# Performance work log

Measured on AMD Instinct MI355X. Metric: run time of the kernel, lower is better.

The kernel has to match this reference:

```python
import jax, jax.numpy as jnp
import numpy as np

B, IN_DIM, OUT_DIM, DEGREE = 4096, 1024, 1024, 4
LN_EPS = 1e-5


def setup_inputs() -> dict:
    key = jax.random.key(0)
    k_x, k_c = jax.random.split(key)
    x = jax.random.normal(k_x, (B, IN_DIM), dtype=jnp.float32)
    # xavier_normal_ on tensor of shape (in, out, deg+1): fan_in/fan_out from
    # torch convention: fan_in = out*(deg+1)? torch computes fan_in=size(1)*receptive,
    # for 3D tensor fan_in = shape[1]*shape[2], fan_out = shape[0]*shape[2].
    fan_in = OUT_DIM * (DEGREE + 1)
    fan_out = IN_DIM * (DEGREE + 1)
    std = float(np.sqrt(2.0 / (fan_in + fan_out)))
    cheby_coeffs = jax.random.normal(k_c, (IN_DIM, OUT_DIM, DEGREE + 1), dtype=jnp.float32) * std
    ln_weight = jnp.ones((IN_DIM,), dtype=jnp.float32)
    ln_bias = jnp.zeros((IN_DIM,), dtype=jnp.float32)
    return {"x": x, "cheby_coeffs": cheby_coeffs, "ln_weight": ln_weight, "ln_bias": ln_bias}


def _layer_norm(x, w, b):
    mu = jnp.mean(x, axis=-1, keepdims=True)
    var = jnp.mean(jnp.square(x - mu), axis=-1, keepdims=True)
    return (x - mu) * jax.lax.rsqrt(var + LN_EPS) * w + b


def reference(x, cheby_coeffs, ln_weight, ln_bias):
    h = jnp.tanh(_layer_norm(x, ln_weight, ln_bias))  # [B, I]
    # Chebyshev recurrence T0=1, T1=h, T_{n}=2h*T_{n-1}-T_{n-2}
    cheby = [jnp.ones_like(h), h]
    for _ in range(2, DEGREE + 1):
        cheby.append(2.0 * h * cheby[-1] - cheby[-2])
    stacked = jnp.stack(cheby, axis=-1)  # [B, I, D+1]
    y = jnp.einsum('bid,iod->bo', stacked, cheby_coeffs)
    return jax.nn.silu(y)
```

## Files before the change

kernel.cpp:

```cpp
#include <hip/hip_runtime.h>
#include <cstdint>
#include <cstddef>

#define BATCH 4096
#define IDIM 1024
#define ODIM 1024
#define KDIM 4096
#define KHALF 2048

typedef __attribute__((ext_vector_type(8))) short bf16x8;
typedef __attribute__((ext_vector_type(4))) float f32x4;

__device__ __forceinline__ unsigned short f2bf(float f) {
  union { float f; unsigned int u; } v; v.f = f;
  unsigned int r = (v.u + 0x7FFFu + ((v.u >> 16) & 1u)) >> 16;
  return (unsigned short)r;
}
__device__ __forceinline__ float bf2f(unsigned short u) {
  union { unsigned int u; float f; } v; v.u = ((unsigned int)u) << 16;
  return v.f;
}

__device__ __forceinline__ void load_lds16(const void* g, void* l) {
  __builtin_amdgcn_global_load_lds(
      (const __attribute__((address_space(1))) void*)g,
      (__attribute__((address_space(3))) void*)l, 16, 0, 0);
}

__device__ __forceinline__ int sidx(int p, int ii) {
  return p * 64 + ((ii + 4 * (p & 15)) & 63);
}

__global__ __launch_bounds__(256) void prep(
    const float* __restrict__ x, const float* __restrict__ lnw,
    const float* __restrict__ lnb, const float* __restrict__ C,
    unsigned short* __restrict__ A, unsigned short* __restrict__ Bt,
    float* __restrict__ biasPart) {
  __shared__ __align__(16) unsigned short sm[64 * 5 * 64];
  int bid = blockIdx.x;
  int t = threadIdx.x;

  if (bid < BATCH) {
    float* rs = (float*)sm;
    float* rq = ((float*)sm) + 4;
    const float4 v = ((const float4*)(x + (size_t)bid * IDIM))[t];
    float s  = v.x + v.y + v.z + v.w;
    float s2 = v.x * v.x + v.y * v.y + v.z * v.z + v.w * v.w;
#pragma unroll
    for (int off = 32; off > 0; off >>= 1) {
      s  += __shfl_down(s, off);
      s2 += __shfl_down(s2, off);
    }
    int lane = t & 63, wv = t >> 6;
    if (lane == 0) { rs[wv] = s; rq[wv] = s2; }
    __syncthreads();
    float S1 = rs[0] + rs[1] + rs[2] + rs[3];
    float S2 = rq[0] + rq[1] + rq[2] + rq[3];
    float mean = S1 * (1.0f / IDIM);
    float var  = S2 * (1.0f / IDIM) - mean * mean;
    float rstd = rsqrtf(var + 1e-5f);

    const float4 w4 = ((const float4*)lnw)[t];
    const float4 b4 = ((const float4*)lnb)[t];
    float xs[4]  = {v.x, v.y, v.z, v.w};
    float ws4[4] = {w4.x, w4.y, w4.z, w4.w};
    float bs4[4] = {b4.x, b4.y, b4.z, b4.w};

    unsigned short u1[4], u2[4], u3[4], u4[4];
#pragma unroll
    for (int j = 0; j < 4; j++) {
      float h  = tanhf((xs[j] - mean) * rstd * ws4[j] + bs4[j]);
      float T2 = 2.0f * h * h - 1.0f;
      float T3 = 2.0f * h * T2 - h;
      float T4 = 2.0f * h * T3 - T2;
      u1[j] = f2bf(h); u2[j] = f2bf(T2); u3[j] = f2bf(T3); u4[j] = f2bf(T4);
    }
    size_t base = (size_t)bid * KDIM;
    *(ushort4*)(A + base + 0 * IDIM + t * 4) = *(ushort4*)u1;
    *(ushort4*)(A + base + 1 * IDIM + t * 4) = *(ushort4*)u2;
    *(ushort4*)(A + base + 2 * IDIM + t * 4) = *(ushort4*)u3;
    *(ushort4*)(A + base + 3 * IDIM + t * 4) = *(ushort4*)u4;
  } else {
    int cb = bid - BATCH;
    int i0 = (cb & 15) * 64, o0 = (cb >> 4) * 64;
#pragma unroll
    for (int r = 0; r < 20; r++) {
      int idx = r * 256 + t;
      int ii  = idx / 80;
      int c4  = idx - ii * 80;
      const float4 f = *(const float4*)(C + ((size_t)(i0 + ii) * ODIM + o0) * 5 + c4 * 4);
      float vals[4] = {f.x, f.y, f.z, f.w};
#pragma unroll
      for (int j = 0; j < 4; j++) {
        int p = c4 * 4 + j;
        sm[sidx(p, ii)] = f2bf(vals[j]);
      }
    }
    __syncthreads();
#pragma unroll
    for (int r = 0; r < 16; r++) {
      int idx = r * 256 + t;
      int seg = idx >> 4, l16 = idx & 15;
      int oo = seg >> 2, d2 = seg & 3;
      int p = oo * 5 + d2 + 1;
      const unsigned short* src = &sm[sidx(p, l16 * 4)];
      ushort4 u = *(const ushort4*)src;
      *(ushort4*)(Bt + (size_t)(o0 + oo) * KDIM + d2 * IDIM + i0 + l16 * 4) = u;
    }
    if (t < 64) {
      float s = 0.f;
      int p = t * 5;
#pragma unroll
      for (int ii = 0; ii < 64; ii++) s += bf2f(sm[sidx(p, ii)]);
      biasPart[(size_t)(i0 >> 6) * ODIM + o0 + t] = s;
    }
  }
}

#define BM 128
#define BN 128
#define BK 64

__global__ __launch_bounds__(256, 2) void gemm_part(
    const unsigned short* __restrict__ A,
    const unsigned short* __restrict__ Bt,
    const float* __restrict__ biasPart,
    float* __restrict__ out0,
    float* __restrict__ part1) {
  __shared__ unsigned short As[BM * BK];
  __shared__ unsigned short Bs[BN * BK];
  int t = threadIdx.x;
  int lane = t & 63, w = t >> 6;
  int m0 = blockIdx.x * BM;
  int n0 = blockIdx.y * BN;
  size_t kbase = (size_t)blockIdx.z * KHALF;

  f32x4 acc[4][4];
#pragma unroll
  for (int i = 0; i < 4; i++)
#pragma unroll
    for (int j = 0; j < 4; j++) acc[i][j] = (f32x4){0.f, 0.f, 0.f, 0.f};

  int wm = (w >> 1) * 64;
  int wn = (w & 1) * 64;

  int sr = lane >> 3;
  int sc = ((lane & 7) ^ sr) * 8;
  const unsigned short* ag[4]; unsigned short* al[4];
  const unsigned short* bg[4]; unsigned short* bl[4];
#pragma unroll
  for (int q = 0; q < 4; q++) {
    int row = w * 8 + q * 32;
    ag[q] = A  + (size_t)(m0 + row + sr) * KDIM + kbase + sc;
    al[q] = &As[row * BK];
    bg[q] = Bt + (size_t)(n0 + row + sr) * KDIM + kbase + sc;
    bl[q] = &Bs[row * BK];
  }

  int arow = (wm + (lane & 15)) * BK;
  int brow = (wn + (lane & 15)) * BK;
  int x7 = lane & 7, hi = lane >> 4;

  for (int k0 = 0; k0 < KHALF; k0 += BK) {
#pragma unroll
    for (int q = 0; q < 4; q++) load_lds16(ag[q] + k0, al[q]);
#pragma unroll
    for (int q = 0; q < 4; q++) load_lds16(bg[q] + k0, bl[q]);
    __syncthreads();
#pragma unroll
    for (int kk = 0; kk < 2; kk++) {
      int co = ((kk * 4 + hi) ^ x7) * 8;
      bf16x8 af[4], bfv[4];
#pragma unroll
      for (int i = 0; i < 4; i++) af[i]  = *(const bf16x8*)&As[arow + i * 16 * BK + co];
#pragma unroll
      for (int j = 0; j < 4; j++) bfv[j] = *(const bf16x8*)&Bs[brow + j * 16 * BK + co];
#pragma unroll
      for (int i = 0; i < 4; i++)
#pragma unroll
        for (int j = 0; j < 4; j++)
          acc[i][j] = __builtin_amdgcn_mfma_f32_16x16x32_bf16(af[i], bfv[j], acc[i][j], 0, 0, 0);
    }
    __syncthreads();
  }

  float* dst = (blockIdx.z == 0) ? out0 : part1;
  bool addb = (blockIdx.z == 0);
#pragma unroll
  for (int j = 0; j < 4; j++) {
    int col = n0 + wn + j * 16 + (lane & 15);
    float bc = 0.f;
    if (addb) {
#pragma unroll
      for (int ib = 0; ib < 16; ib++) bc += biasPart[(size_t)ib * ODIM + col];
    }
#pragma unroll
    for (int i = 0; i < 4; i++) {
      int row = m0 + wm + i * 16 + hi * 4;
#pragma unroll
      for (int r = 0; r < 4; r++)
        dst[(size_t)(row + r) * ODIM + col] = acc[i][j][r] + bc;
    }
  }
}

__global__ __launch_bounds__(256) void reduce_silu(
    float* __restrict__ out, const float* __restrict__ part1) {
  int idx = blockIdx.x * 256 + threadIdx.x;
  float4 a = ((const float4*)out)[idx];
  float4 b = ((const float4*)part1)[idx];
  float y0 = a.x + b.x, y1 = a.y + b.y, y2 = a.z + b.z, y3 = a.w + b.w;
  float4 o;
  o.x = y0 / (1.0f + __expf(-y0));
  o.y = y1 / (1.0f + __expf(-y1));
  o.z = y2 / (1.0f + __expf(-y2));
  o.w = y3 / (1.0f + __expf(-y3));
  ((float4*)out)[idx] = o;
}

extern "C" void kernel_launch(void* const* d_in, const int* in_sizes, int n_in,
                              void* d_out, int out_size, void* d_ws, size_t ws_size,
                              hipStream_t stream) {
  const float* x    = (const float*)d_in[0];
  const float* coef = (const float*)d_in[1];
  const float* lnw  = (const float*)d_in[2];
  const float* lnb  = (const float*)d_in[3];
  float* out = (float*)d_out;

  char* ws = (char*)d_ws;
  unsigned short* A  = (unsigned short*)ws;
  unsigned short* Bt = (unsigned short*)(ws + (size_t)BATCH * KDIM * 2);
  char* p = ws + (size_t)BATCH * KDIM * 2 + (size_t)ODIM * KDIM * 2;
  float* biasPart = (float*)p;
  float* part1 = (float*)(p + 16 * ODIM * sizeof(float));

  prep<<<BATCH + 256, 256, 0, stream>>>(x, lnw, lnb, coef, A, Bt, biasPart);
  gemm_part<<<dim3(BATCH / BM, ODIM / BN, 2), 256, 0, stream>>>(A, Bt, biasPart, out, part1);
  reduce_silu<<<(BATCH * ODIM) / (256 * 4), 256, 0, stream>>>(out, part1);
}
```

Baseline: 138.9 us.

## Double-buffer LDS tiles in split-K GEMM to overlap global loads with MFMA

The GEMM main loop now uses two LDS buffers per operand. It issues the global-to-LDS loads for the next K tile before computing on the current one, so memory latency overlaps with MFMA work instead of stalling at each barrier. This doubles LDS use per block to 64KB, which may limit occupancy for the two-blocks-per-CU launch bound. Correctness depends on the __syncthreads making the async global_load_lds data visible, since there is no explicit vmcnt wait.

```diff
diff --git a/kernel.cpp b/kernel.cpp
--- a/kernel.cpp
+++ b/kernel.cpp
@@ -120,6 +120,7 @@
 #define BM 128
 #define BN 128
 #define BK 64
+#define NIT (KHALF / BK)
 
 __global__ __launch_bounds__(256, 2) void gemm_part(
     const unsigned short* __restrict__ A,
@@ -127,8 +128,8 @@
     const float* __restrict__ biasPart,
     float* __restrict__ out0,
     float* __restrict__ part1) {
-  __shared__ unsigned short As[BM * BK];
-  __shared__ unsigned short Bs[BN * BK];
+  __shared__ unsigned short As[2 * BM * BK];
+  __shared__ unsigned short Bs[2 * BN * BK];
   int t = threadIdx.x;
   int lane = t & 63, w = t >> 6;
   int m0 = blockIdx.x * BM;
@@ -161,27 +162,43 @@
   int brow = (wn + (lane & 15)) * BK;
   int x7 = lane & 7, hi = lane >> 4;
 
-  for (int k0 = 0; k0 < KHALF; k0 += BK) {
-#pragma unroll
-    for (int q = 0; q < 4; q++) load_lds16(ag[q] + k0, al[q]);
-#pragma unroll
-    for (int q = 0; q < 4; q++) load_lds16(bg[q] + k0, bl[q]);
-    __syncthreads();
-#pragma unroll
-    for (int kk = 0; kk < 2; kk++) {
-      int co = ((kk * 4 + hi) ^ x7) * 8;
-      bf16x8 af[4], bfv[4];
-#pragma unroll
-      for (int i = 0; i < 4; i++) af[i]  = *(const bf16x8*)&As[arow + i * 16 * BK + co];
-#pragma unroll
-      for (int j = 0; j < 4; j++) bfv[j] = *(const bf16x8*)&Bs[brow + j * 16 * BK + co];
-#pragma unroll
-      for (int i = 0; i < 4; i++)
-#pragma unroll
-        for (int j = 0; j < 4; j++)
-          acc[i][j] = __builtin_amdgcn_mfma_f32_16x16x32_bf16(af[i], bfv[j], acc[i][j], 0, 0, 0);
-    }
-    __syncthreads();
+#define ISSUE(buf, kk0)                                                     \
+  do {                                                                      \
+    int _k = (kk0);                                                         \
+    _Pragma("unroll")                                                       \
+    for (int q = 0; q < 4; q++) load_lds16(ag[q] + _k, al[q] + (buf) * (BM * BK)); \
+    _Pragma("unroll")                                                       \
+    for (int q = 0; q < 4; q++) load_lds16(bg[q] + _k, bl[q] + (buf) * (BN * BK)); \
+  } while (0)
+
+#define COMPUTE(buf)                                                        \
+  do {                                                                      \
+    _Pragma("unroll")                                                       \
+    for (int kk = 0; kk < 2; kk++) {                                        \
+      int co = ((kk * 4 + hi) ^ x7) * 8;                                    \
+      bf16x8 af[4], bfv[4];                                                 \
+      _Pragma("unroll")                                                     \
+      for (int i = 0; i < 4; i++)                                           \
+        af[i]  = *(const bf16x8*)&As[(buf) * (BM * BK) + arow + i * 16 * BK + co]; \
+      _Pragma("unroll")                                                     \
+      for (int j = 0; j < 4; j++)                                           \
+        bfv[j] = *(const bf16x8*)&Bs[(buf) * (BN * BK) + brow + j * 16 * BK + co]; \
+      _Pragma("unroll")                                                     \
+      for (int i = 0; i < 4; i++)                                           \
+        _Pragma("unroll")                                                   \
+        for (int j = 0; j < 4; j++)                                         \
+          acc[i][j] = __builtin_amdgcn_mfma_f32_16x16x32_bf16(af[i], bfv[j], acc[i][j], 0, 0, 0); \
+    }                                                                       \
+  } while (0)
+
+  ISSUE(0, 0);
+  for (int it = 0; it < NIT; it += 2) {
+    __syncthreads();
+    if (it + 1 < NIT) ISSUE(1, (it + 1) * BK);
+    COMPUTE(0);
+    __syncthreads();
+    if (it + 2 < NIT) ISSUE(0, (it + 2) * BK);
+    COMPUTE(1);
   }
 
   float* dst = (blockIdx.z == 0) ? out0 : part1;
```

Result: no change. 138.4 us (-0.3%).

## Double-buffer GEMM mainloop with per-wave B tiles and direct-to-register A loads

Applied to the files above, without the earlier changes.

Replaces the block-shared LDS tiles and the two __syncthreads per k-step with a per-wave, double-buffered B tile in LDS, fed by global_load_lds. A fragments are loaded straight from global memory into registers. An explicit vmcnt wait lets the next tile's loads overlap the current tile's MFMAs without block-level barriers. The cost is duplicated B loads across waves, less coalesced A reads, 64KB of LDS per block, and higher register pressure from buffered A fragments.

```diff
diff --git a/kernel.cpp b/kernel.cpp
--- a/kernel.cpp
+++ b/kernel.cpp
@@ -120,6 +120,9 @@
 #define BM 128
 #define BN 128
 #define BK 64
+#define NIT (KHALF / BK)
+
+#define WAIT_VM16() __builtin_amdgcn_s_waitcnt(0x4F70)
 
 __global__ __launch_bounds__(256, 2) void gemm_part(
     const unsigned short* __restrict__ A,
@@ -127,61 +130,82 @@
     const float* __restrict__ biasPart,
     float* __restrict__ out0,
     float* __restrict__ part1) {
-  __shared__ unsigned short As[BM * BK];
-  __shared__ unsigned short Bs[BN * BK];
+  __shared__ unsigned short Bs[4][2][64 * BK];
   int t = threadIdx.x;
   int lane = t & 63, w = t >> 6;
   int m0 = blockIdx.x * BM;
   int n0 = blockIdx.y * BN;
   size_t kbase = (size_t)blockIdx.z * KHALF;
-
-  f32x4 acc[4][4];
-#pragma unroll
-  for (int i = 0; i < 4; i++)
-#pragma unroll
-    for (int j = 0; j < 4; j++) acc[i][j] = (f32x4){0.f, 0.f, 0.f, 0.f};
-
   int wm = (w >> 1) * 64;
   int wn = (w & 1) * 64;
 
+  f32x4 acc[4][4];
+#pragma unroll
+  for (int i = 0; i < 4; i++)
+#pragma unroll
+    for (int j = 0; j < 4; j++) acc[i][j] = (f32x4){0.f, 0.f, 0.f, 0.f};
+
   int sr = lane >> 3;
   int sc = ((lane & 7) ^ sr) * 8;
-  const unsigned short* ag[4]; unsigned short* al[4];
-  const unsigned short* bg[4]; unsigned short* bl[4];
-#pragma unroll
-  for (int q = 0; q < 4; q++) {
-    int row = w * 8 + q * 32;
-    ag[q] = A  + (size_t)(m0 + row + sr) * KDIM + kbase + sc;
-    al[q] = &As[row * BK];
-    bg[q] = Bt + (size_t)(n0 + row + sr) * KDIM + kbase + sc;
-    bl[q] = &Bs[row * BK];
-  }
-
-  int arow = (wm + (lane & 15)) * BK;
-  int brow = (wn + (lane & 15)) * BK;
+  const unsigned short* bg[8];
+  unsigned short* bl[8];
+#pragma unroll
+  for (int q = 0; q < 8; q++) {
+    int row = q * 8;
+    bg[q] = Bt + (size_t)(n0 + wn + row + sr) * KDIM + kbase + sc;
+    bl[q] = &Bs[w][0][row * BK];
+  }
+
+  const unsigned short* ar[4];
+#pragma unroll
+  for (int i = 0; i < 4; i++)
+    ar[i] = A + (size_t)(m0 + wm + i * 16 + (lane & 15)) * KDIM + kbase + (lane >> 4) * 8;
+
   int x7 = lane & 7, hi = lane >> 4;
-
-  for (int k0 = 0; k0 < KHALF; k0 += BK) {
-#pragma unroll
-    for (int q = 0; q < 4; q++) load_lds16(ag[q] + k0, al[q]);
-#pragma unroll
-    for (int q = 0; q < 4; q++) load_lds16(bg[q] + k0, bl[q]);
-    __syncthreads();
-#pragma unroll
-    for (int kk = 0; kk < 2; kk++) {
-      int co = ((kk * 4 + hi) ^ x7) * 8;
-      bf16x8 af[4], bfv[4];
-#pragma unroll
-      for (int i = 0; i < 4; i++) af[i]  = *(const bf16x8*)&As[arow + i * 16 * BK + co];
-#pragma unroll
-      for (int j = 0; j < 4; j++) bfv[j] = *(const bf16x8*)&Bs[brow + j * 16 * BK + co];
-#pragma unroll
-      for (int i = 0; i < 4; i++)
-#pragma unroll
-        for (int j = 0; j < 4; j++)
-          acc[i][j] = __builtin_amdgcn_mfma_f32_16x16x32_bf16(af[i], bfv[j], acc[i][j], 0, 0, 0);
-    }
-    __syncthreads();
+  int brw = (lane & 15) * BK;
+
+  bf16x8 afr[2][2][4];
+
+#define ISSUE(buf, kk0)                                                      \
+  do {                                                                       \
+    int _k = (kk0);                                                          \
+    _Pragma("unroll")                                                        \
+    for (int q = 0; q < 8; q++)                                              \
+      load_lds16(bg[q] + _k, bl[q] + (buf) * (64 * BK));                     \
+    _Pragma("unroll")                                                        \
+    for (int kk = 0; kk < 2; kk++)                                           \
+      _Pragma("unroll")                                                      \
+      for (int i = 0; i < 4; i++)                                            \
+        afr[buf][kk][i] = *(const bf16x8*)(ar[i] + _k + kk * 32);            \
+  } while (0)
+
+#define COMPUTE(buf)                                                         \
+  do {                                                                       \
+    WAIT_VM16();                                                             \
+    _Pragma("unroll")                                                        \
+    for (int kk = 0; kk < 2; kk++) {                                         \
+      int co = ((kk * 4 + hi) ^ x7) * 8;                                     \
+      bf16x8 bfv[4];                                                         \
+      _Pragma("unroll")                                                      \
+      for (int j = 0; j < 4; j++)                                            \
+        bfv[j] = *(const bf16x8*)&Bs[w][buf][brw + j * 16 * BK + co];        \
+      _Pragma("unroll")                                                      \
+      for (int i = 0; i < 4; i++)                                            \
+        _Pragma("unroll")                                                    \
+        for (int j = 0; j < 4; j++)                                          \
+          acc[i][j] = __builtin_amdgcn_mfma_f32_16x16x32_bf16(              \
+              afr[buf][kk][i], bfv[j], acc[i][j], 0, 0, 0);                  \
+    }                                                                        \
+  } while (0)
+
+  ISSUE(0, 0);
+  for (int it = 0; it < NIT; it += 2) {
+    int k1 = (it + 1 < NIT) ? (it + 1) * BK : (NIT - 1) * BK;
+    ISSUE(1, k1);
+    COMPUTE(0);
+    int k2 = (it + 2 < NIT) ? (it + 2) * BK : (NIT - 1) * BK;
+    ISSUE(0, k2);
+    COMPUTE(1);
   }
 
   float* dst = (blockIdx.z == 0) ? out0 : part1;
```

Result: slower. 179.0 us (+28.9%).
